# Kernel tuning notes

Hardware: AMD Instinct MI355X
Metric: run time of the kernel (lower is better)

The kernel has to match this reference:

```python
import jax, jax.numpy as jnp
import numpy as np

B, S, D = 2, 2048, 768
H = 12
HD = D // H


def setup_inputs() -> dict:
    key = jax.random.key(0)
    k1, k2, k3 = jax.random.split(key, 3)
    hidden_states = jax.random.normal(k1, (B, S, D), dtype=jnp.float32)
    Wqkv = jax.random.normal(k2, (D, 3 * D), dtype=jnp.float32) * (1.0 / np.sqrt(D))
    bqkv = jnp.zeros((3 * D,), dtype=jnp.float32)
    Wout = jax.random.normal(k3, (D, D), dtype=jnp.float32) * (1.0 / np.sqrt(D))
    bout = jnp.zeros((D,), dtype=jnp.float32)
    return {"hidden_states": hidden_states, "Wqkv": Wqkv, "bqkv": bqkv,
            "Wout": Wout, "bout": bout}


def reference(hidden_states, Wqkv, bqkv, Wout, bout):
    b, s, d = hidden_states.shape
    h, hd = H, HD
    scale = hd ** -0.5
    qkv = hidden_states @ Wqkv + bqkv                      # [b, s, 3d]
    q, k, v = jnp.split(qkv, 3, axis=-1)
    # [b, h, s, hd]
    q = q.reshape(b, s, h, hd).transpose(0, 2, 1, 3)
    k = k.reshape(b, s, h, hd).transpose(0, 2, 1, 3)
    v = v.reshape(b, s, h, hd).transpose(0, 2, 1, 3)
    scores = jnp.einsum('bhqd,bhkd->bhqk', q, k) * scale   # [b, h, s, s]
    causal = jnp.tril(jnp.ones((s, s), dtype=bool))
    scores = jnp.where(causal, scores, -jnp.inf)
    attn = jax.nn.softmax(scores, axis=-1)
    out = jnp.einsum('bhqk,bhkd->bhqd', attn, v)           # [b, h, s, hd]
    out = out.transpose(0, 2, 1, 3).reshape(b, s, d)
    return out @ Wout + bout
```

## Files before the change

### kernel.cpp

```cpp
#include <hip/hip_runtime.h>
#include <hip/hip_bf16.h>

typedef __attribute__((ext_vector_type(8))) short bf16x8;
typedef __attribute__((ext_vector_type(4))) float f32x4;
typedef __attribute__((ext_vector_type(4))) unsigned int u32x4;

#define NB 2
#define NS 2048
#define ND 768
#define NH 12
#define NHD 64
#define N3D 2304
#define NM (NB * NS)

__device__ __forceinline__ unsigned short f2bf(float x) {
    union { float f; unsigned u; } v; v.f = x;
    unsigned r = v.u + 0x7FFFu + ((v.u >> 16) & 1u);
    return (unsigned short)(r >> 16);
}

__device__ __forceinline__ unsigned cvt_pk_bf16(float lo, float hi) {
    unsigned r;
    asm volatile("v_cvt_pk_bf16_f32 %0, %1, %2" : "=v"(r) : "v"(lo), "v"(hi));
    return r;
}

__device__ __forceinline__ float fexp2(float x) {
    float r;
    asm("v_exp_f32 %0, %1" : "=v"(r) : "v"(x));
    return r;
}

__device__ __forceinline__ void transp_tile(const float* __restrict__ in,
                                            unsigned short* __restrict__ out,
                                            int K, int N, int nt, int kt,
                                            float (*T)[33]) {
    const int n0 = nt * 32, k0 = kt * 32;
    const int r = threadIdx.x >> 3, c4 = (threadIdx.x & 7) * 4;
    float4 v = *reinterpret_cast<const float4*>(&in[(size_t)(k0 + r) * N + n0 + c4]);
    T[r][c4 + 0] = v.x; T[r][c4 + 1] = v.y; T[r][c4 + 2] = v.z; T[r][c4 + 3] = v.w;
    __syncthreads();
    ushort4 o;
    o.x = f2bf(T[c4 + 0][r]); o.y = f2bf(T[c4 + 1][r]);
    o.z = f2bf(T[c4 + 2][r]); o.w = f2bf(T[c4 + 3][r]);
    *reinterpret_cast<ushort4*>(&out[(size_t)(n0 + r) * K + k0 + c4]) = o;
}

__global__ __launch_bounds__(256)
void prep(const float* __restrict__ hs, unsigned short* __restrict__ hsb,
          const float* __restrict__ Wqkv, unsigned short* __restrict__ W1t,
          const float* __restrict__ Wout, unsigned short* __restrict__ W2t) {
    __shared__ float T[32][33];
    const int bid = blockIdx.x;
    if (bid < 3072) {
        const int i = (bid * 256 + threadIdx.x) * 4;
        float4 v = *reinterpret_cast<const float4*>(hs + i);
        ushort4 o;
        o.x = f2bf(v.x); o.y = f2bf(v.y); o.z = f2bf(v.z); o.w = f2bf(v.w);
        *reinterpret_cast<ushort4*>(hsb + i) = o;
    } else if (bid < 3072 + 1728) {
        const int idx = bid - 3072;
        transp_tile(Wqkv, W1t, ND, N3D, idx % 72, idx / 72, T);
    } else {
        const int idx = bid - 4800;
        transp_tile(Wout, W2t, ND, ND, idx % 24, idx / 24, T);
    }
}

template<int BM, int BN, int EPI>
__global__ __launch_bounds__(256)
void gemm_k768(const unsigned short* __restrict__ A,
               const unsigned short* __restrict__ Bt,
               const float* __restrict__ bias,
               unsigned short* __restrict__ Qo, unsigned short* __restrict__ Ko,
               unsigned short* __restrict__ Vto, float* __restrict__ Co) {
    __shared__ unsigned short SMEM[(BM + BN) * 64];
    unsigned short* As = SMEM;
    unsigned short* Bs = SMEM + BM * 64;
    const int t = threadIdx.x;
    const int wv = t >> 6, lane = t & 63;
    const int lr = lane & 15, lg = lane >> 4;
    const int wr = wv >> 1, wc = wv & 1;
    const int m0 = blockIdx.y * BM;
    const int n0 = blockIdx.x * BN;
    constexpr int FM = BM / 32;
    constexpr int FN = BN / 32;

    f32x4 acc[FM][FN];
#pragma unroll
    for (int i = 0; i < FM; ++i)
#pragma unroll
        for (int j = 0; j < FN; ++j) acc[i][j] = (f32x4){0.f, 0.f, 0.f, 0.f};

    const int sr = t >> 3;
    const int sb = t & 7;

    for (int ki = 0; ki < ND / 64; ++ki) {
        const int k0 = ki * 64;
        __syncthreads();
#pragma unroll
        for (int jj = 0; jj < BM / 32; ++jj) {
            const int row = jj * 32 + sr;
            __builtin_amdgcn_global_load_lds(
                (const void*)(A + (size_t)(m0 + row) * ND + k0 + ((sb ^ (row & 7)) * 8)),
                (void*)(As + jj * 2048 + wv * 512), 16, 0, 0);
        }
#pragma unroll
        for (int jj = 0; jj < BN / 32; ++jj) {
            const int row = jj * 32 + sr;
            __builtin_amdgcn_global_load_lds(
                (const void*)(Bt + (size_t)(n0 + row) * ND + k0 + ((sb ^ (row & 7)) * 8)),
                (void*)(Bs + jj * 2048 + wv * 512), 16, 0, 0);
        }
        __syncthreads();
#pragma unroll
        for (int kc = 0; kc < 2; ++kc) {
            bf16x8 af[FM], bfr[FN];
#pragma unroll
            for (int mi = 0; mi < FM; ++mi) {
                const int row = wr * (BM / 2) + mi * 16 + lr;
                af[mi] = *(const bf16x8*)&As[row * 64 + (((kc * 4 + lg) ^ (row & 7)) * 8)];
            }
#pragma unroll
            for (int nj = 0; nj < FN; ++nj) {
                const int row = wc * (BN / 2) + nj * 16 + lr;
                bfr[nj] = *(const bf16x8*)&Bs[row * 64 + (((kc * 4 + lg) ^ (row & 7)) * 8)];
            }
#pragma unroll
            for (int mi = 0; mi < FM; ++mi)
#pragma unroll
                for (int nj = 0; nj < FN; ++nj)
                    acc[mi][nj] = __builtin_amdgcn_mfma_f32_16x16x32_bf16(
                        af[mi], bfr[nj], acc[mi][nj], 0, 0, 0);
        }
    }

    if (EPI == 0) {
        const int sec = n0 / ND;
        if (sec < 2) {
#pragma unroll
            for (int mi = 0; mi < FM; ++mi) {
#pragma unroll
                for (int nj = 0; nj < FN; ++nj) {
                    const int n = n0 + wc * (BN / 2) + nj * 16 + lr;
                    const int rem = n - sec * ND;
                    const int hh = rem >> 6, dd = rem & 63;
                    const float b = bias[n];
#pragma unroll
                    for (int r = 0; r < 4; ++r) {
                        const int m = m0 + wr * (BM / 2) + mi * 16 + lg * 4 + r;
                        const int bb = m >> 11, ss = m & (NS - 1);
                        const int bhh = bb * NH + hh;
                        const float v = acc[mi][nj][r] + b;
                        if (sec == 0)
                            Qo[((size_t)bhh * NS + ss) * NHD + dd] = f2bf(v * 0.18033688011112042f);
                        else
                            Ko[((size_t)bhh * NS + ss) * NHD + dd] = f2bf(v);
                    }
                }
            }
        } else {
            __syncthreads();
            char* Tb = reinterpret_cast<char*>(SMEM);
#pragma unroll
            for (int mi = 0; mi < FM; ++mi) {
#pragma unroll
                for (int nj = 0; nj < FN; ++nj) {
                    const int n_l = wc * (BN / 2) + nj * 16 + lr;
                    const int m_l = wr * (BM / 2) + mi * 16 + lg * 4;
                    const float b = bias[n0 + n_l];
                    ushort4 pk;
                    pk.x = f2bf(acc[mi][nj][0] + b);
                    pk.y = f2bf(acc[mi][nj][1] + b);
                    pk.z = f2bf(acc[mi][nj][2] + b);
                    pk.w = f2bf(acc[mi][nj][3] + b);
                    const int off = n_l * 256 + (((m_l * 2) ^ ((n_l & 15) << 4)));
                    *reinterpret_cast<ushort4*>(Tb + off) = pk;
                }
            }
            __syncthreads();
            const int bb = m0 >> 11;
            const int ssb = m0 & (NS - 1);
#pragma unroll
            for (int h = 0; h < (BN * 16) / 256; ++h) {
                const int pp = t + 256 * h;
                const int n_l = pp >> 4, j = pp & 15;
                const int off = n_l * 256 + (((j ^ (n_l & 15)) << 4));
                bf16x8 v = *reinterpret_cast<const bf16x8*>(Tb + off);
                const int rem = n0 + n_l - 2 * ND;
                const int hh = rem >> 6, dd = rem & 63;
                const int bhh = bb * NH + hh;
                *reinterpret_cast<bf16x8*>(Vto + ((size_t)(bhh * NHD + dd)) * NS + ssb + 8 * j) = v;
            }
        }
    } else {
#pragma unroll
        for (int mi = 0; mi < FM; ++mi)
#pragma unroll
            for (int nj = 0; nj < FN; ++nj) {
                const int n = n0 + wc * (BN / 2) + nj * 16 + lr;
                const float b = bias[n];
#pragma unroll
                for (int r = 0; r < 4; ++r) {
                    const int m = m0 + wr * (BM / 2) + mi * 16 + lg * 4 + r;
                    Co[(size_t)m * ND + n] = acc[mi][nj][r] + b;
                }
            }
    }
}

__global__ __launch_bounds__(256)
void attn_mfma(const unsigned short* __restrict__ Qg,
               const unsigned short* __restrict__ Kg,
               const unsigned short* __restrict__ Vtg,
               unsigned short* __restrict__ AO) {
    __shared__ unsigned short Ks[2][128 * 64];
    __shared__ unsigned short Vs[64 * 128];
    float* MRG = reinterpret_cast<float*>(Vs);

    const int n = blockIdx.x;
    const int x = n & 7, ii = n >> 3;
    const int bh = ((ii >> 5) << 3) + x;
    const int jp = ii & 31;
    const int t = threadIdx.x;
    const int w = t >> 6, lane = t & 63;
    const int lr = lane & 15, lg = lane >> 4;
    const int lgp = lg & 1;
    const int qh = w & 1, p = w >> 1;
    const size_t bhoff = (size_t)bh * (NS * NHD);
    const unsigned short* Kb = Kg + bhoff;
    const unsigned short* Vb = Vtg + bhoff;
    const int bswz = ((lg & 1) << 1) | (lg >> 1);
    const int ksr = lane >> 3, ksb = lane & 7;
    const int vsr = lane >> 4, vsb = lane & 15;
    const int bb = bh / NH, hh = bh - bb * NH;

#define STAGEK(buf, kvb)                                                        \
    {                                                                           \
        _Pragma("unroll")                                                       \
        for (int g = 0; g < 4; ++g) {                                           \
            const int row = g * 32 + w * 8 + ksr;                               \
            __builtin_amdgcn_global_load_lds(                                   \
                (const void*)(Kb + (size_t)((kvb) + row) * NHD + ((ksb ^ (row & 7)) * 8)), \
                (void*)(Ks[buf] + (g * 32 + w * 8) * 64), 16, 0, 0);            \
        }                                                                       \
    }
#define STAGEV(kvb)                                                             \
    {                                                                           \
        _Pragma("unroll")                                                       \
        for (int g = 0; g < 4; ++g) {                                           \
            const int d = g * 16 + w * 4 + vsr;                                 \
            __builtin_amdgcn_global_load_lds(                                   \
                (const void*)(Vb + (size_t)d * NS + (kvb) + ((vsb ^ (d & 7)) * 8)), \
                (void*)(Vs + (g * 16 + w * 4) * 128), 16, 0, 0);                \
        }                                                                       \
    }

#pragma unroll 1
    for (int mem = 0; mem < 2; ++mem) {
        const int qtile = mem ? jp : 63 - jp;
        const int q0 = qtile * 32;
        const int nr = qtile / 4 + 1;
        const int qrow = q0 + qh * 16 + lr;

        const unsigned short* Qp = Qg + bhoff + (size_t)qrow * NHD;
        const bf16x8 qB0 = *(const bf16x8*)(Qp + lg * 8);
        const bf16x8 qB1 = *(const bf16x8*)(Qp + 32 + lg * 8);

        float m_run = -1e30f, l_part = 0.f;
        f32x4 of[4];
#pragma unroll
        for (int f = 0; f < 4; ++f) of[f] = (f32x4){0.f, 0.f, 0.f, 0.f};

        STAGEK(0, 0);
        __syncthreads();
#pragma unroll 1
        for (int R = 0; R < nr; ++R) {
            STAGEV(R * 128);
            if (R + 1 < nr) STAGEK((R + 1) & 1, (R + 1) * 128);
            const unsigned short* Kc = Ks[R & 1];
            const int kvw = R * 128 + p * 64;
            const bool active = kvw <= q0 + 31;

            f32x4 sf[4];
            bf16x8 pb[2];
            if (active) {
#pragma unroll
                for (int f = 0; f < 4; ++f) sf[f] = (f32x4){0.f, 0.f, 0.f, 0.f};
                __builtin_amdgcn_s_setprio(1);
#pragma unroll
                for (int f = 0; f < 4; ++f) {
                    const int krow = p * 64 + f * 16 + lr;
                    const bf16x8 a0 = *(const bf16x8*)&Kc[krow * 64 + ((lg ^ (krow & 7)) * 8)];
                    const bf16x8 a1 = *(const bf16x8*)&Kc[krow * 64 + (((4 + lg) ^ (krow & 7)) * 8)];
                    sf[f] = __builtin_amdgcn_mfma_f32_16x16x32_bf16(a0, qB0, sf[f], 0, 0, 0);
                    sf[f] = __builtin_amdgcn_mfma_f32_16x16x32_bf16(a1, qB1, sf[f], 0, 0, 0);
                }
                __builtin_amdgcn_s_setprio(0);

                const int rel = qrow - kvw;
                if (rel < 63) {
#pragma unroll
                    for (int f = 0; f < 4; ++f)
#pragma unroll
                        for (int r = 0; r < 4; ++r)
                            if (f * 16 + lg * 4 + r > rel) sf[f][r] = -1e30f;
                }

                float tm = -1e30f;
#pragma unroll
                for (int f = 0; f < 4; ++f)
                    tm = fmaxf(tm, fmaxf(fmaxf(sf[f][0], sf[f][1]), fmaxf(sf[f][2], sf[f][3])));
                tm = fmaxf(tm, __shfl_xor(tm, 16));
                tm = fmaxf(tm, __shfl_xor(tm, 32));
                if (!__all(tm <= m_run)) {
                    const float nm = fmaxf(m_run, tm);
                    const float corr = fexp2(m_run - nm);
                    m_run = nm;
                    l_part *= corr;
#pragma unroll
                    for (int f = 0; f < 4; ++f)
#pragma unroll
                        for (int r = 0; r < 4; ++r) of[f][r] *= corr;
                }
#pragma unroll
                for (int f = 0; f < 4; ++f)
#pragma unroll
                    for (int r = 0; r < 4; ++r) {
                        sf[f][r] = fexp2(sf[f][r] - m_run);
                        l_part += sf[f][r];
                    }

#pragma unroll
                for (int c = 0; c < 2; ++c) {
                    const unsigned A0 = cvt_pk_bf16(sf[2 * c][0], sf[2 * c][1]);
                    const unsigned A1 = cvt_pk_bf16(sf[2 * c][2], sf[2 * c][3]);
                    const unsigned B0 = cvt_pk_bf16(sf[2 * c + 1][0], sf[2 * c + 1][1]);
                    const unsigned B1 = cvt_pk_bf16(sf[2 * c + 1][2], sf[2 * c + 1][3]);
                    const unsigned s0 = lgp ? A0 : B0;
                    const unsigned s1 = lgp ? A1 : B1;
                    const unsigned r0 = (unsigned)__shfl_xor((int)s0, 16);
                    const unsigned r1 = (unsigned)__shfl_xor((int)s1, 16);
                    const unsigned o0 = lgp ? B0 : A0;
                    const unsigned o1 = lgp ? B1 : A1;
                    u32x4 wvv;
                    wvv[0] = lgp ? r0 : o0;
                    wvv[1] = lgp ? r1 : o1;
                    wvv[2] = lgp ? o0 : r0;
                    wvv[3] = lgp ? o1 : r1;
                    pb[c] = __builtin_bit_cast(bf16x8, wvv);
                }
            }
            __syncthreads();
            if (active) {
                __builtin_amdgcn_s_setprio(1);
#pragma unroll
                for (int fA = 0; fA < 4; ++fA) {
                    const int drow = fA * 16 + lr;
#pragma unroll
                    for (int c = 0; c < 2; ++c) {
                        const int blk = p * 8 + 4 * c + bswz;
                        const bf16x8 va = *(const bf16x8*)&Vs[drow * 128 + ((blk ^ (drow & 7)) * 8)];
                        of[fA] = __builtin_amdgcn_mfma_f32_16x16x32_bf16(va, pb[c], of[fA], 0, 0, 0);
                    }
                }
                __builtin_amdgcn_s_setprio(0);
            }
            __syncthreads();
        }

        l_part += __shfl_xor(l_part, 16);
        l_part += __shfl_xor(l_part, 32);
        if (p == 1) {
            float* mr = &MRG[(qh * 64 + lane) * 18];
            mr[0] = m_run; mr[1] = l_part;
#pragma unroll
            for (int f = 0; f < 4; ++f)
#pragma unroll
                for (int r = 0; r < 4; ++r) mr[2 + f * 4 + r] = of[f][r];
        }
        __syncthreads();
        if (p == 0) {
            const float* mr = &MRG[(qh * 64 + lane) * 18];
            const float m1 = mr[0], l1 = mr[1];
            const float mm = fmaxf(m_run, m1);
            const float a0 = fexp2(m_run - mm);
            const float a1 = fexp2(m1 - mm);
            const float inv = 1.f / (l_part * a0 + l1 * a1);
            unsigned short* op = AO + ((size_t)(bb * NS + qrow)) * ND + hh * NHD;
#pragma unroll
            for (int fA = 0; fA < 4; ++fA) {
                ushort4 o4;
                o4.x = f2bf((of[fA][0] * a0 + mr[2 + fA * 4 + 0] * a1) * inv);
                o4.y = f2bf((of[fA][1] * a0 + mr[2 + fA * 4 + 1] * a1) * inv);
                o4.z = f2bf((of[fA][2] * a0 + mr[2 + fA * 4 + 2] * a1) * inv);
                o4.w = f2bf((of[fA][3] * a0 + mr[2 + fA * 4 + 3] * a1) * inv);
                *reinterpret_cast<ushort4*>(op + fA * 16 + lg * 4) = o4;
            }
        }
        __syncthreads();
    }
#undef STAGEK
#undef STAGEV
}

extern "C" void kernel_launch(void* const* d_in, const int* in_sizes, int n_in,
                              void* d_out, int out_size, void* d_ws, size_t ws_size,
                              hipStream_t stream) {
    const float* hs   = (const float*)d_in[0];
    const float* Wqkv = (const float*)d_in[1];
    const float* bqkv = (const float*)d_in[2];
    const float* Wout = (const float*)d_in[3];
    const float* bout = (const float*)d_in[4];
    float* out = (float*)d_out;

    char* wp = (char*)d_ws;
    unsigned short* hsb = (unsigned short*)wp; wp += (size_t)NM * ND * 2;
    unsigned short* W1t = (unsigned short*)wp; wp += (size_t)N3D * ND * 2;
    unsigned short* W2t = (unsigned short*)wp; wp += (size_t)ND * ND * 2;
    const size_t per = (size_t)NB * NH * NS * NHD;
    unsigned short* Qb  = (unsigned short*)wp; wp += per * 2;
    unsigned short* Kb  = (unsigned short*)wp; wp += per * 2;
    unsigned short* Vtb = (unsigned short*)wp; wp += per * 2;
    unsigned short* AOb = (unsigned short*)wp; wp += per * 2;

    prep<<<3072 + 1728 + 576, 256, 0, stream>>>(hs, hsb, Wqkv, W1t, Wout, W2t);

    gemm_k768<128, 96, 0><<<dim3(N3D / 96, NM / 128), 256, 0, stream>>>(
        hsb, W1t, bqkv, Qb, Kb, Vtb, nullptr);

    attn_mfma<<<768, 256, 0, stream>>>(Qb, Kb, Vtb, AOb);

    gemm_k768<64, 64, 1><<<dim3(ND / 64, NM / 64), 256, 0, stream>>>(
        AOb, W2t, bout, nullptr, nullptr, nullptr, out);
}
```

Baseline: 155.3 us.

## Hold K tiles in registers and double-buffer V in LDS

The attention kernel no longer stages K through shared memory. Each wave loads its own K fragments straight from global memory into registers, prefetching the next tile after the QK MFMAs. The shared buffer now double-buffers V instead, which drops one barrier per iteration and overlaps the V load with compute. The output projection GEMM tile also changes from 64x64 to 64x96. The trade-off is higher register pressure and K reads from global with no reuse across waves.

```diff
diff --git a/kernel.cpp b/kernel.cpp
--- a/kernel.cpp
+++ b/kernel.cpp
@@ -214,9 +214,8 @@
                const unsigned short* __restrict__ Kg,
                const unsigned short* __restrict__ Vtg,
                unsigned short* __restrict__ AO) {
-    __shared__ unsigned short Ks[2][128 * 64];
-    __shared__ unsigned short Vs[64 * 128];
-    float* MRG = reinterpret_cast<float*>(Vs);
+    __shared__ unsigned short Vs[2][64 * 128];
+    float* MRG = reinterpret_cast<float*>(Vs[0]);
 
     const int n = blockIdx.x;
     const int x = n & 7, ii = n >> 3;
@@ -231,28 +230,28 @@
     const unsigned short* Kb = Kg + bhoff;
     const unsigned short* Vb = Vtg + bhoff;
     const int bswz = ((lg & 1) << 1) | (lg >> 1);
-    const int ksr = lane >> 3, ksb = lane & 7;
     const int vsr = lane >> 4, vsb = lane & 15;
     const int bb = bh / NH, hh = bh - bb * NH;
 
-#define STAGEK(buf, kvb)                                                        \
+    bf16x8 kK[4][2];
+
+#define LOADK(kvb)                                                              \
     {                                                                           \
         _Pragma("unroll")                                                       \
-        for (int g = 0; g < 4; ++g) {                                           \
-            const int row = g * 32 + w * 8 + ksr;                               \
-            __builtin_amdgcn_global_load_lds(                                   \
-                (const void*)(Kb + (size_t)((kvb) + row) * NHD + ((ksb ^ (row & 7)) * 8)), \
-                (void*)(Ks[buf] + (g * 32 + w * 8) * 64), 16, 0, 0);            \
-        }                                                                       \
-    }
-#define STAGEV(kvb)                                                             \
+        for (int f = 0; f < 4; ++f)                                             \
+            _Pragma("unroll")                                                   \
+            for (int c = 0; c < 2; ++c)                                         \
+                kK[f][c] = *(const bf16x8*)(Kb +                                \
+                    (size_t)((kvb) + p * 64 + f * 16 + lr) * NHD + c * 32 + lg * 8); \
+    }
+#define STAGEV(buf, kvb)                                                        \
     {                                                                           \
         _Pragma("unroll")                                                       \
         for (int g = 0; g < 4; ++g) {                                           \
             const int d = g * 16 + w * 4 + vsr;                                 \
             __builtin_amdgcn_global_load_lds(                                   \
                 (const void*)(Vb + (size_t)d * NS + (kvb) + ((vsb ^ (d & 7)) * 8)), \
-                (void*)(Vs + (g * 16 + w * 4) * 128), 16, 0, 0);                \
+                (void*)(Vs[buf] + (g * 16 + w * 4) * 128), 16, 0, 0);           \
         }                                                                       \
     }
 
@@ -272,13 +271,13 @@
 #pragma unroll
         for (int f = 0; f < 4; ++f) of[f] = (f32x4){0.f, 0.f, 0.f, 0.f};
 
-        STAGEK(0, 0);
+        LOADK(0);
+        STAGEV(0, 0);
         __syncthreads();
 #pragma unroll 1
         for (int R = 0; R < nr; ++R) {
-            STAGEV(R * 128);
-            if (R + 1 < nr) STAGEK((R + 1) & 1, (R + 1) * 128);
-            const unsigned short* Kc = Ks[R & 1];
+            if (R + 1 < nr) STAGEV((R + 1) & 1, (R + 1) * 128);
+            const unsigned short* Vc = Vs[R & 1];
             const int kvw = R * 128 + p * 64;
             const bool active = kvw <= q0 + 31;
 
@@ -290,14 +289,13 @@
                 __builtin_amdgcn_s_setprio(1);
 #pragma unroll
                 for (int f = 0; f < 4; ++f) {
-                    const int krow = p * 64 + f * 16 + lr;
-                    const bf16x8 a0 = *(const bf16x8*)&Kc[krow * 64 + ((lg ^ (krow & 7)) * 8)];
-                    const bf16x8 a1 = *(const bf16x8*)&Kc[krow * 64 + (((4 + lg) ^ (krow & 7)) * 8)];
-                    sf[f] = __builtin_amdgcn_mfma_f32_16x16x32_bf16(a0, qB0, sf[f], 0, 0, 0);
-                    sf[f] = __builtin_amdgcn_mfma_f32_16x16x32_bf16(a1, qB1, sf[f], 0, 0, 0);
+                    sf[f] = __builtin_amdgcn_mfma_f32_16x16x32_bf16(kK[f][0], qB0, sf[f], 0, 0, 0);
+                    sf[f] = __builtin_amdgcn_mfma_f32_16x16x32_bf16(kK[f][1], qB1, sf[f], 0, 0, 0);
                 }
                 __builtin_amdgcn_s_setprio(0);
-
+            }
+            if (R + 1 < nr) LOADK((R + 1) * 128);
+            if (active) {
                 const int rel = qrow - kvw;
                 if (rel < 63) {
 #pragma unroll
@@ -350,9 +348,7 @@
                     wvv[3] = lgp ? o1 : r1;
                     pb[c] = __builtin_bit_cast(bf16x8, wvv);
                 }
-            }
-            __syncthreads();
-            if (active) {
+
                 __builtin_amdgcn_s_setprio(1);
 #pragma unroll
                 for (int fA = 0; fA < 4; ++fA) {
@@ -360,7 +356,7 @@
 #pragma unroll
                     for (int c = 0; c < 2; ++c) {
                         const int blk = p * 8 + 4 * c + bswz;
-                        const bf16x8 va = *(const bf16x8*)&Vs[drow * 128 + ((blk ^ (drow & 7)) * 8)];
+                        const bf16x8 va = *(const bf16x8*)&Vc[drow * 128 + ((blk ^ (drow & 7)) * 8)];
                         of[fA] = __builtin_amdgcn_mfma_f32_16x16x32_bf16(va, pb[c], of[fA], 0, 0, 0);
                     }
                 }
@@ -400,7 +396,7 @@
         }
         __syncthreads();
     }
-#undef STAGEK
+#undef LOADK
 #undef STAGEV
 }
 
@@ -431,6 +427,6 @@
 
     attn_mfma<<<768, 256, 0, stream>>>(Qb, Kb, Vtb, AOb);
 
-    gemm_k768<64, 64, 1><<<dim3(ND / 64, NM / 64), 256, 0, stream>>>(
+    gemm_k768<64, 96, 1><<<dim3(ND / 96, NM / 64), 256, 0, stream>>>(
         AOb, W2t, bout, nullptr, nullptr, nullptr, out);
 }
```

After: 181.5 us. +16.9%, slower.
